# Performance work log

Measured on AMD Instinct MI355X. Metric: run time of the kernel, lower is better.

## Reference

```python
import jax, jax.numpy as jnp
import numpy as np

N = 50000          # num nodes
E = 800000         # num edges (avg degree 16)
F_IN = 512         # num_feature
HID = 128          # hid
COM_LAMBDA = 1.0


def setup_inputs() -> dict:
    key = jax.random.key(0)
    k1, k2, k3, k4, k5, k6 = jax.random.split(key, 6)
    v_ori_vals = jax.random.uniform(k1, (E,), dtype=jnp.float32)
    feat = jax.random.normal(k2, (N, F_IN), dtype=jnp.float32)
    v_indices = jax.random.randint(k3, (2, E), 0, N, dtype=jnp.int64)
    # GraphConvolution params
    gcn_w = jax.random.normal(k4, (F_IN, HID), dtype=jnp.float32) / np.sqrt(F_IN)
    gcn_b = jnp.zeros((HID,), dtype=jnp.float32)
    # gen_mlp: Linear(2*hid, 1), xavier_normal init
    std = 1.414 * np.sqrt(2.0 / (2 * HID + 1))
    mlp_w = jax.random.normal(k5, (1, 2 * HID), dtype=jnp.float32) * std
    mlp_b = jnp.zeros((1,), dtype=jnp.float32)
    return {"v_ori_vals": v_ori_vals, "feat": feat, "v_indices": v_indices,
            "num_node": N, "gcn_w": gcn_w, "gcn_b": gcn_b,
            "mlp_w": mlp_w, "mlp_b": mlp_b}


def reference(v_ori_vals, feat, v_indices, num_node, gcn_w, gcn_b, mlp_w, mlp_b):
    row, col = v_indices[0], v_indices[1]
    # gen_gcn: emb = A @ (feat @ W) + b  (SpMM via segment_sum over edges)
    support = feat @ gcn_w                                      # [N, HID]
    emb = jax.ops.segment_sum(v_ori_vals[:, None] * support[col], row,
                              num_segments=num_node) + gcn_b    # [N, HID]
    # gather endpoints, concat, edge-scoring MLP (dropout = identity in eval)
    ff = jnp.concatenate([emb[row], emb[col]], axis=-1)         # [E, 2*HID]
    temp = (ff @ mlp_w.T + mlp_b).reshape(-1)                   # [E]
    # sparse row-wise softmax over columns (dim=1) -> segment softmax by row
    m = jax.ops.segment_max(temp, row, num_segments=num_node)   # [N]
    e = jnp.exp(temp - m[row])                                  # [E]
    s = jax.ops.segment_sum(e, row, num_segments=num_node)      # [N]
    pi = e / s[row]                                             # [E]
    # gen_v = v_ori + com_lambda * pi (values on the shared edge pattern)
    return v_ori_vals + COM_LAMBDA * pi
```

## Files before the change

### kernel.cpp

```cpp
#include <hip/hip_runtime.h>


typedef unsigned int u32;

#define RPB     128
#define CAP     3072
#define NB_MAX  512
#define SB      256
#define GB      782

__global__ void k_prep(const float* __restrict__ W, const float* __restrict__ mw,
                       float* __restrict__ u2, u32* __restrict__ cnt,
                       int F, int H, int nb) {
  if (blockIdx.x == 0)
    for (int s = threadIdx.x; s < nb; s += blockDim.x) cnt[s] = 0;
  int f = blockIdx.x * blockDim.x + threadIdx.x;
  if (f >= F) return;
  const float4* wr = (const float4*)(W + (size_t)f * H);
  const float4* mv = (const float4*)(mw + H);
  float s = 0.f;
  for (int i = 0; i < H / 4; ++i) {
    float4 a = wr[i], b = mv[i];
    s = fmaf(a.x, b.x, fmaf(a.y, b.y, fmaf(a.z, b.z, fmaf(a.w, b.w, s))));
  }
  u2[f] = s;
}

template <int F>
__global__ void __launch_bounds__(1024)
k_fused(const int* __restrict__ row, const int* __restrict__ col,
        const float* __restrict__ v, const float* __restrict__ feat,
        const float* __restrict__ u2, float* __restrict__ q,
        u32* __restrict__ cnt, uint2* __restrict__ rec8,
        int E, int N, int nb) {
  __shared__ u32 h[NB_MAX];
  __shared__ u32 start[NB_MAX];
  const int tid = threadIdx.x;

  if (blockIdx.x < SB) {
    const int chunk = (E + SB - 1) / SB;
    for (int s = tid; s < nb; s += blockDim.x) h[s] = 0;
    __syncthreads();
    const int lo = blockIdx.x * chunk;
    const int hi = min(E, lo + chunk);
    for (int e = lo + tid; e < hi; e += blockDim.x)
      atomicAdd(&h[row[e] >> 7], 1u);
    __syncthreads();
    for (int s = tid; s < nb; s += blockDim.x) {
      u32 c = h[s];
      start[s] = c ? atomicAdd(&cnt[s], c) : 0u;
      h[s] = 0u;
    }
    __syncthreads();
    for (int e = lo + tid; e < hi; e += blockDim.x) {
      int r = row[e];
      int b = r >> 7;
      u32 rank = atomicAdd(&h[b], 1u);
      u32 off  = min(start[b] + rank, (u32)CAP - 1);
      rec8[(size_t)b * CAP + off] =
          make_uint2(((u32)col[e] << 7) | (u32)(r & 127),
                     __float_as_uint(v[e]));
    }
  } else {
    const int lane = tid & 63;
    const float4 ua = *(const float4*)(u2 + lane * 8);
    const float4 ub = *(const float4*)(u2 + lane * 8 + 4);
    const int wid = (blockIdx.x - SB) * (1024 >> 6) + (tid >> 6);
    const int nw  = GB * (1024 >> 6);
    for (int r = wid; r < N; r += nw) {
      const float* fr = feat + (size_t)r * F + lane * 8;
      float4 a = *(const float4*)fr;
      float4 b = *(const float4*)(fr + 4);
      float s = fmaf(a.x, ua.x, fmaf(a.y, ua.y, fmaf(a.z, ua.z,
                fmaf(a.w, ua.w, fmaf(b.x, ub.x, fmaf(b.y, ub.y,
                fmaf(b.z, ub.z, b.w * ub.w)))))));
      s += __shfl_xor(s, 32);
      s += __shfl_xor(s, 16);
      s += __shfl_xor(s, 8);
      s += __shfl_xor(s, 4);
      s += __shfl_xor(s, 2);
      s += __shfl_xor(s, 1);
      if (lane == 0) q[r] = s;
    }
  }
}

__global__ void __launch_bounds__(1024)
k_sum_t(const uint2* __restrict__ rec8, const u32* __restrict__ cnt,
        const float* __restrict__ q, float* __restrict__ t) {
  __shared__ float acc[RPB];
  const int b = blockIdx.x;
  const int tid = threadIdx.x;
  if (tid < RPB) acc[tid] = 0.f;
  __syncthreads();
  const u32 lo = (u32)b * CAP;
  const u32 n  = min(cnt[b], (u32)CAP);
  for (u32 i = tid; i < n; i += blockDim.x) {
    uint2 rr = rec8[lo + i];
    atomicAdd(&acc[rr.x & 127], q[rr.x >> 7] * __uint_as_float(rr.y));
  }
  __syncthreads();
  if (tid < RPB) t[b * RPB + tid] = __expf(acc[tid]);
}

__global__ void __launch_bounds__(1024)
k_sum_invS(const uint2* __restrict__ rec8, const u32* __restrict__ cnt,
           const float* __restrict__ t, float* __restrict__ invS) {
  __shared__ float acc[RPB];
  const int b = blockIdx.x;
  const int tid = threadIdx.x;
  if (tid < RPB) acc[tid] = 0.f;
  __syncthreads();
  const u32 lo = (u32)b * CAP;
  const u32 n  = min(cnt[b], (u32)CAP);
  for (u32 i = tid; i < n; i += blockDim.x) {
    uint2 rr = rec8[lo + i];
    atomicAdd(&acc[rr.x & 127], t[rr.x >> 7]);
  }
  __syncthreads();
  if (tid < RPB) invS[b * RPB + tid] = 1.0f / acc[tid];
}

__global__ void k_out(const int* __restrict__ row, const int* __restrict__ col,
                      const float* __restrict__ vori, const float* __restrict__ t,
                      const float* __restrict__ invS, float* __restrict__ out,
                      int E) {
  int e4 = blockIdx.x * blockDim.x + threadIdx.x;
  int e  = e4 * 4;
  if (e + 3 < E) {
    int4   r4 = *(const int4*)(row + e);
    int4   c4 = *(const int4*)(col + e);
    float4 v4 = *(const float4*)(vori + e);
    float4 o;
    o.x = v4.x + t[c4.x] * invS[r4.x];
    o.y = v4.y + t[c4.y] * invS[r4.y];
    o.z = v4.z + t[c4.z] * invS[r4.z];
    o.w = v4.w + t[c4.w] * invS[r4.w];
    *(float4*)(out + e) = o;
  } else {
    for (; e < E; ++e)
      out[e] = vori[e] + t[col[e]] * invS[row[e]];
  }
}

__global__ void k_gemv_fb(const float* __restrict__ feat, const float* __restrict__ u2,
                          float* __restrict__ q, int N, int F) {
  const int lane = threadIdx.x & 63;
  const int wave = (blockIdx.x * blockDim.x + threadIdx.x) >> 6;
  if (wave >= N) return;
  const float* fr = feat + (size_t)wave * F;
  float a = 0.f;
  for (int i = lane; i < F; i += 64) a = fmaf(fr[i], u2[i], a);
  for (int off = 32; off; off >>= 1) a += __shfl_xor(a, off);
  if (lane == 0) q[wave] = a;
}
__global__ void k_scatter_B_at(const int* __restrict__ row, const int* __restrict__ col,
                               const float* __restrict__ v, const float* __restrict__ q,
                               float* __restrict__ B, int E) {
  int e = blockIdx.x * blockDim.x + threadIdx.x;
  if (e >= E) return;
  atomicAdd(&B[row[e]], v[e] * q[col[e]]);
}
__global__ void k_node_t(const float* __restrict__ B, float* __restrict__ t, int N) {
  int n = blockIdx.x * blockDim.x + threadIdx.x;
  if (n < N) t[n] = __expf(B[n]);
}
__global__ void k_scatter_S_at(const int* __restrict__ row, const int* __restrict__ col,
                               const float* __restrict__ t, float* __restrict__ S, int E) {
  int e = blockIdx.x * blockDim.x + threadIdx.x;
  if (e >= E) return;
  atomicAdd(&S[row[e]], t[col[e]]);
}
__global__ void k_out_div(const int* __restrict__ row, const int* __restrict__ col,
                          const float* __restrict__ vori, const float* __restrict__ t,
                          const float* __restrict__ S, float* __restrict__ out, int E) {
  int e = blockIdx.x * blockDim.x + threadIdx.x;
  if (e >= E) return;
  out[e] = vori[e] + t[col[e]] / S[row[e]];
}

extern "C" void kernel_launch(void* const* d_in, const int* in_sizes, int n_in,
                              void* d_out, int out_size, void* d_ws, size_t ws_size,
                              hipStream_t stream) {
  const float* vori = (const float*)d_in[0];
  const float* feat = (const float*)d_in[1];
  const int*   vind = (const int*)d_in[2];
  const float* W    = (const float*)d_in[4];
  const float* mw   = (const float*)d_in[6];

  const int E = in_sizes[0];
  const int H = in_sizes[6] / 2;
  const int F = in_sizes[4] / H;
  const int N = in_sizes[1] / F;

  const int* row = vind;
  const int* col = vind + E;

  const int nb   = (N + RPB - 1) / RPB;
  const int npad = nb * RPB;

  float* ws   = (float*)d_ws;
  float* u2   = ws;
  float* q    = u2 + F;
  float* t    = q + N;
  float* invS = t + npad;
  u32*   cnt  = (u32*)(invS + npad);
  size_t hdr  = (size_t)((char*)(cnt + nb) - (char*)d_ws);
  hdr = (hdr + 15) & ~(size_t)15;
  uint2* rec8 = (uint2*)((char*)d_ws + hdr);
  size_t need = hdr + (size_t)nb * CAP * sizeof(uint2);

  k_prep<<<(F + 255) / 256, 256, 0, stream>>>(W, mw, u2, cnt, F, H, nb);

  if (ws_size >= need && F == 512 && H % 4 == 0 && nb <= NB_MAX) {
    k_fused<512><<<SB + GB, 1024, 0, stream>>>(row, col, vori, feat, u2, q,
                                               cnt, rec8, E, N, nb);
    k_sum_t<<<nb, 1024, 0, stream>>>(rec8, cnt, q, t);
    k_sum_invS<<<nb, 1024, 0, stream>>>(rec8, cnt, t, invS);
    const int e4 = (E + 3) / 4;
    k_out<<<(e4 + 255) / 256, 256, 0, stream>>>(row, col, vori, t, invS,
                                                (float*)d_out, E);
  } else {
    const int eb  = (E + 255) / 256;
    const int nbk = (N + 255) / 256;
    float* S = invS;
    k_gemv_fb<<<(N * 64 + 255) / 256, 256, 0, stream>>>(feat, u2, q, N, F);
    hipMemsetAsync((void*)S, 0, sizeof(float) * (size_t)npad, stream);
    k_scatter_B_at<<<eb, 256, 0, stream>>>(row, col, vori, q, S, E);
    k_node_t<<<nbk, 256, 0, stream>>>(S, t, N);
    hipMemsetAsync((void*)S, 0, sizeof(float) * (size_t)npad, stream);
    k_scatter_S_at<<<eb, 256, 0, stream>>>(row, col, t, S, E);
    k_out_div<<<eb, 256, 0, stream>>>(row, col, vori, t, S, (float*)d_out, E);
  }
}
```

Measured before the change: 207.8 us.

## Balance fused bucketing and GEMV work with dynamic row chunks, pad counters

Instead of splitting blocks statically into bucketing blocks and GEMV blocks, the fused kernel now launches fewer blocks. Every block, including the bucketing ones once they finish, pulls 16-row chunks of the feat·u2 GEMV from a global atomic dispatcher. Per-bucket counters are padded to separate 64-byte lines to cut false sharing on the global atomics. This trades a static partition for dynamic load balancing, at the cost of one atomic per chunk and a larger zeroing pass in the prep kernel.

```diff
diff --git a/kernel.cpp b/kernel.cpp
--- a/kernel.cpp
+++ b/kernel.cpp
@@ -6,14 +6,16 @@
 #define RPB     128
 #define CAP     3072
 #define NB_MAX  512
+#define CPAD    16
 #define SB      256
-#define GB      782
+#define FG      512
+#define GCHUNK  16
 
 __global__ void k_prep(const float* __restrict__ W, const float* __restrict__ mw,
                        float* __restrict__ u2, u32* __restrict__ cnt,
-                       int F, int H, int nb) {
+                       int F, int H, int nz) {
   if (blockIdx.x == 0)
-    for (int s = threadIdx.x; s < nb; s += blockDim.x) cnt[s] = 0;
+    for (int s = threadIdx.x; s < nz; s += blockDim.x) cnt[s] = 0;
   int f = blockIdx.x * blockDim.x + threadIdx.x;
   if (f >= F) return;
   const float4* wr = (const float4*)(W + (size_t)f * H);
@@ -31,56 +33,63 @@
 k_fused(const int* __restrict__ row, const int* __restrict__ col,
         const float* __restrict__ v, const float* __restrict__ feat,
         const float* __restrict__ u2, float* __restrict__ q,
-        u32* __restrict__ cnt, uint2* __restrict__ rec8,
-        int E, int N, int nb) {
+        u32* __restrict__ cnt, u32* __restrict__ disp,
+        uint2* __restrict__ rec8, int E, int N, int nb) {
   __shared__ u32 h[NB_MAX];
   __shared__ u32 start[NB_MAX];
-  const int tid = threadIdx.x;
+  const int tid  = threadIdx.x;
+  const int lane = tid & 63;
 
   if (blockIdx.x < SB) {
     const int chunk = (E + SB - 1) / SB;
-    for (int s = tid; s < nb; s += blockDim.x) h[s] = 0;
+    for (int s = tid; s < nb; s += 1024) h[s] = 0;
     __syncthreads();
     const int lo = blockIdx.x * chunk;
     const int hi = min(E, lo + chunk);
-    for (int e = lo + tid; e < hi; e += blockDim.x)
+    for (int e = lo + tid; e < hi; e += 1024)
       atomicAdd(&h[row[e] >> 7], 1u);
     __syncthreads();
-    for (int s = tid; s < nb; s += blockDim.x) {
+    for (int s = tid; s < nb; s += 1024) {
       u32 c = h[s];
-      start[s] = c ? atomicAdd(&cnt[s], c) : 0u;
+      start[s] = c ? atomicAdd(&cnt[(size_t)s * CPAD], c) : 0u;
       h[s] = 0u;
     }
     __syncthreads();
-    for (int e = lo + tid; e < hi; e += blockDim.x) {
+    for (int e = lo + tid; e < hi; e += 1024) {
       int r = row[e];
       int b = r >> 7;
       u32 rank = atomicAdd(&h[b], 1u);
-      u32 off  = min(start[b] + rank, (u32)CAP - 1);
+      u32 off  = min(start[b] + rank, (u32)(CAP - 1));
       rec8[(size_t)b * CAP + off] =
           make_uint2(((u32)col[e] << 7) | (u32)(r & 127),
                      __float_as_uint(v[e]));
     }
-  } else {
-    const int lane = tid & 63;
+  }
+
+  {
     const float4 ua = *(const float4*)(u2 + lane * 8);
     const float4 ub = *(const float4*)(u2 + lane * 8 + 4);
-    const int wid = (blockIdx.x - SB) * (1024 >> 6) + (tid >> 6);
-    const int nw  = GB * (1024 >> 6);
-    for (int r = wid; r < N; r += nw) {
-      const float* fr = feat + (size_t)r * F + lane * 8;
-      float4 a = *(const float4*)fr;
-      float4 b = *(const float4*)(fr + 4);
-      float s = fmaf(a.x, ua.x, fmaf(a.y, ua.y, fmaf(a.z, ua.z,
-                fmaf(a.w, ua.w, fmaf(b.x, ub.x, fmaf(b.y, ub.y,
-                fmaf(b.z, ub.z, b.w * ub.w)))))));
-      s += __shfl_xor(s, 32);
-      s += __shfl_xor(s, 16);
-      s += __shfl_xor(s, 8);
-      s += __shfl_xor(s, 4);
-      s += __shfl_xor(s, 2);
-      s += __shfl_xor(s, 1);
-      if (lane == 0) q[r] = s;
+    for (;;) {
+      u32 base = 0;
+      if (lane == 0) base = atomicAdd(disp, (u32)GCHUNK);
+      base = __shfl(base, 0);
+      if (base >= (u32)N) break;
+      const u32 end = min(base + (u32)GCHUNK, (u32)N);
+      for (u32 r = base; r < end; ++r) {
+        const float* fr = feat + (size_t)r * F + lane * 8;
+        float4 a = *(const float4*)fr;
+        float4 b = *(const float4*)(fr + 4);
+        float s = fmaf(a.x, ua.x, fmaf(a.y, ua.y, fmaf(a.z, ua.z,
+                  fmaf(a.w, ua.w, fmaf(b.x, ub.x, fmaf(b.y, ub.y,
+                  fmaf(b.z, ub.z, b.w * ub.w)))))));
+        s += __shfl_xor(s, 32);
+        s += __shfl_xor(s, 16);
+        s += __shfl_xor(s, 8);
+        s += __shfl_xor(s, 4);
+        s += __shfl_xor(s, 2);
+        s += __shfl_xor(s, 1);
+        if (lane == 0) q[r] = s;
+      }
     }
   }
 }
@@ -94,7 +103,7 @@
   if (tid < RPB) acc[tid] = 0.f;
   __syncthreads();
   const u32 lo = (u32)b * CAP;
-  const u32 n  = min(cnt[b], (u32)CAP);
+  const u32 n  = min(cnt[(size_t)b * CPAD], (u32)CAP);
   for (u32 i = tid; i < n; i += blockDim.x) {
     uint2 rr = rec8[lo + i];
     atomicAdd(&acc[rr.x & 127], q[rr.x >> 7] * __uint_as_float(rr.y));
@@ -112,7 +121,7 @@
   if (tid < RPB) acc[tid] = 0.f;
   __syncthreads();
   const u32 lo = (u32)b * CAP;
-  const u32 n  = min(cnt[b], (u32)CAP);
+  const u32 n  = min(cnt[(size_t)b * CPAD], (u32)CAP);
   for (u32 i = tid; i < n; i += blockDim.x) {
     uint2 rr = rec8[lo + i];
     atomicAdd(&acc[rr.x & 127], t[rr.x >> 7]);
@@ -205,16 +214,18 @@
   float* t    = q + N;
   float* invS = t + npad;
   u32*   cnt  = (u32*)(invS + npad);
-  size_t hdr  = (size_t)((char*)(cnt + nb) - (char*)d_ws);
-  hdr = (hdr + 15) & ~(size_t)15;
+  u32*   disp = cnt + (size_t)nb * CPAD;
+  size_t hdr  = (size_t)((char*)(disp + 16) - (char*)d_ws);
+  hdr = (hdr + 63) & ~(size_t)63;
   uint2* rec8 = (uint2*)((char*)d_ws + hdr);
   size_t need = hdr + (size_t)nb * CAP * sizeof(uint2);
 
-  k_prep<<<(F + 255) / 256, 256, 0, stream>>>(W, mw, u2, cnt, F, H, nb);
+  k_prep<<<(F + 255) / 256, 256, 0, stream>>>(W, mw, u2, cnt, F, H,
+                                              nb * CPAD + 16);
 
   if (ws_size >= need && F == 512 && H % 4 == 0 && nb <= NB_MAX) {
-    k_fused<512><<<SB + GB, 1024, 0, stream>>>(row, col, vori, feat, u2, q,
-                                               cnt, rec8, E, N, nb);
+    k_fused<512><<<FG, 1024, 0, stream>>>(row, col, vori, feat, u2, q,
+                                          cnt, disp, rec8, E, N, nb);
     k_sum_t<<<nb, 1024, 0, stream>>>(rec8, cnt, q, t);
     k_sum_invS<<<nb, 1024, 0, stream>>>(rec8, cnt, t, invS);
     const int e4 = (E + 3) / 4;
```

Measured after the change: 307.8 us. 1.48x slower.
